# Performance work log

Hardware: AMD Instinct MI355X
Metric: run time of the kernel (lower is better)

## Reference

```python
import jax, jax.numpy as jnp
import numpy as np

# Arbitrary non-contiguous kernel tap offsets (constructor arg sk_ind)
SK_IND = np.array([-512, -256, -128, -96, -64, -48, -32, -24, -16, -12, -8, -6,
                   -4, -3, -2, -1, 0, 1, 2, 3, 4, 6, 8, 12, 16, 24, 32, 48,
                   64, 96, 128, 256], dtype=np.int32)
IN_CHANNELS = 64
OUT_CHANNELS = 64
BATCH = 16
INPUT_LEN = 4096


def setup_inputs() -> dict:
    key = jax.random.key(0)
    k1, k2 = jax.random.split(key)
    x = jax.random.normal(k1, (BATCH, IN_CHANNELS, INPUT_LEN), dtype=jnp.float32)
    sk_weights = jax.random.normal(k2, (OUT_CHANNELS, IN_CHANNELS, SK_IND.shape[0]), dtype=jnp.float32)
    return {"x": x, "sk_weights": sk_weights}


def reference(x, sk_weights):
    # x: [B, Cin, L]; sk_weights: [Cout, Cin, K]
    B, C, L = x.shape
    low_pad = max(-int(SK_IND.min()), 0)   # zeros consumed by negative taps
    high_pad = max(int(SK_IND.max()), 0)   # zeros consumed by positive taps
    # Original pads zeros AFTER the signal: [x, zeros(high_pad), zeros(low_pad)];
    # negative numpy indices then wrap into the trailing low_pad zeros.
    padded = jnp.concatenate([x, jnp.zeros((B, C, high_pad + low_pad), x.dtype)], axis=-1)
    padded_len = L + high_pad + low_pad
    idx = SK_IND[:, None] + np.arange(L)                 # [K, L], static
    idx = np.where(idx < 0, padded_len + idx, idx)       # emulate numpy negative-index wrap
    gathered = padded[:, :, idx]                          # [B, Cin, K, L]
    # Per-position GEMM: contract over (Cin, K)
    return jnp.einsum('oik,bikl->bol', sk_weights, gathered)  # [B, Cout, L]
```

## Files before the change

### kernel.cpp

```cpp
#include <hip/hip_runtime.h>


#define B_    16
#define CIN   64
#define COUT  64
#define LEN   4096
#define PAD_LO 512
#define PAD_HI 256
#define LPAD  (LEN + PAD_LO + PAD_HI)
#define NTAP  32

typedef float f32x4 __attribute__((ext_vector_type(4)));
typedef short bf16x8_s __attribute__((ext_vector_type(8)));
typedef __bf16 bf16x8_b __attribute__((ext_vector_type(8)));
typedef unsigned short u16x8 __attribute__((ext_vector_type(8)));

template <typename V>
static __device__ inline auto mfma_16x16x32_bf16(V a, V b, f32x4 c, int)
    -> decltype(__builtin_amdgcn_mfma_f32_16x16x32_bf16(a, b, c, 0, 0, 0)) {
  return __builtin_amdgcn_mfma_f32_16x16x32_bf16(a, b, c, 0, 0, 0);
}
template <typename V>
static __device__ inline f32x4 mfma_16x16x32_bf16(V a, V b, f32x4 c, long) {
  return __builtin_amdgcn_mfma_f32_16x16x32_bf16(
      __builtin_bit_cast(bf16x8_b, a), __builtin_bit_cast(bf16x8_b, b), c, 0, 0, 0);
}

static __device__ inline unsigned short f32_to_bf16_rne(float f) {
  unsigned int u = __builtin_bit_cast(unsigned int, f);
  u += 0x7fffu + ((u >> 16) & 1u);
  return (unsigned short)(u >> 16);
}

static __device__ inline void async_copy16(const void* g, void* l) {
  __builtin_amdgcn_global_load_lds((const __attribute__((address_space(1))) unsigned int*)g,
                                   (__attribute__((address_space(3))) unsigned int*)l, 16, 0, 0);
}

__global__ __launch_bounds__(256) void prep_xw(const float* __restrict__ x,
                                               const float* __restrict__ w,
                                               unsigned short* __restrict__ xp,
                                               unsigned short* __restrict__ wf) {
  __shared__ float tile[64][65];
  const int b = blockIdx.y;
  const int lp0 = blockIdx.x * 64;
  const int tid = threadIdx.x;
  const bool data = (lp0 >= PAD_LO) && (lp0 < PAD_LO + LEN);
  if (data) {
    const int l0 = lp0 - PAD_LO;
#pragma unroll
    for (int it = 0; it < 4; ++it) {
      const int pidx = it * 256 + tid;
      const int il = pidx >> 4;
      const int lq = (pidx & 15) * 4;
      const float4 v = *(const float4*)&x[(size_t)(b * CIN + il) * LEN + l0 + lq];
      tile[lq + 0][il] = v.x;
      tile[lq + 1][il] = v.y;
      tile[lq + 2][il] = v.z;
      tile[lq + 3][il] = v.w;
    }
  } else if (lp0 < PAD_LO) {
    const int base = (b * 8 + blockIdx.x) * 1024;
#pragma unroll
    for (int it = 0; it < 4; ++it) {
      const int e = base + it * 256 + tid;
      const int j = e & 7;
      const int lane = (e >> 3) & 63;
      const int m = (e >> 9) & 3;
      const int c = (e >> 11) & 1;
      const int t = e >> 12;
      const int o = m * 16 + (lane & 15);
      const int i = c * 32 + (lane >> 4) * 8 + j;
      wf[e] = f32_to_bf16_rne(w[(size_t)(o * CIN + i) * NTAP + t]);
    }
  }
  __syncthreads();
#pragma unroll
  for (int it = 0; it < 2; ++it) {
    const int pidx = it * 256 + tid;
    const int ll = pidx >> 3;
    const int i8 = (pidx & 7) * 8;
    u16x8 v = {0, 0, 0, 0, 0, 0, 0, 0};
    if (data) {
#pragma unroll
      for (int j = 0; j < 8; ++j) v[j] = f32_to_bf16_rne(tile[ll][i8 + j]);
    }
    *(u16x8*)&xp[(size_t)(b * LPAD + lp0 + ll) * CIN + i8] = v;
  }
}

__global__ __launch_bounds__(256, 2) void sconv_main(const unsigned short* __restrict__ xp,
                                                     const unsigned short* __restrict__ wf,
                                                     float* __restrict__ out) {
  constexpr int TAP[NTAP] = {-512, -256, -128, -96, -64, -48, -32, -24, -16, -12, -8,
                             -6,   -4,   -3,   -2,  -1,  0,   1,   2,   3,   4,  6,
                             8,    12,   16,   24,  32,  48,  64,  96,  128, 256};
  constexpr int NCH = 7;
  constexpr int CS[NCH + 1] = {0, 1, 2, 4, 8, 16, 24, 32};
  constexpr int SEND[NCH] = {-385, -129, 31, 103, 126, 135, 383};
  __shared__ alignas(16) char smem[65536];

  const int id = blockIdx.x;
  const int b = (id & 7) * 2 + ((id >> 3) & 1);
  const int l0 = (id >> 4) * 128;
  const int lb = l0 + PAD_LO;
  const int tid = threadIdx.x;
  const int wv = tid >> 6, lane = tid & 63;
  const int q = lane >> 4, r = lane & 15;
  const int lh = wv;

  const char* xbase = (const char*)xp + ((size_t)b * LPAD + lb) * (CIN * 2);
  const char* wbase = (const char*)wf;

  auto stageB = [&](int a0, int ng) {
    for (int g = wv; g < ng; g += 4) {
      const int ra = a0 + g * 8 + (lane >> 3);
      const int cs = (lane & 7) ^ (ra & 7);
      const int sb = (lb + a0 + g * 8) & 511;
      async_copy16(xbase + (ptrdiff_t)ra * 128 + cs * 16, smem + sb * 128);
    }
  };

  bf16x8_s Wreg[2][8], Breg[2][4];
  f32x4 acc[4][2] = {};

  auto loadW = [&](int tt, int p) {
    const char* src = wbase + tt * 8192 + lane * 16;
#pragma unroll
    for (int m = 0; m < 4; ++m)
#pragma unroll
      for (int c = 0; c < 2; ++c)
        Wreg[p][m * 2 + c] = *(const bf16x8_s*)(src + c * 4096 + m * 1024);
  };
  auto readB = [&](int tt, int p) {
    const int e = (TAP[tt] + r) & 7;
#pragma unroll
    for (int n = 0; n < 2; ++n) {
      const int slot = (lb + TAP[tt] + lh * 32 + 16 * n + r) & 511;
#pragma unroll
      for (int c = 0; c < 2; ++c)
        Breg[p][n * 2 + c] = *(const bf16x8_s*)(smem + slot * 128 + (((c * 4 + q) ^ e) << 4));
    }
  };

  loadW(0, 0);
  stageB(-512, 16);

#pragma unroll
  for (int i = 0; i < NCH; ++i) {
    __syncthreads();
    if (i + 1 < NCH) {
      const int ds = SEND[i] + 1;
      const int a0 = ds & ~7;
      stageB(a0, (SEND[i + 1] + 1 - a0 + 7) >> 3);
    }
    __builtin_amdgcn_sched_barrier(0);
    readB(CS[i], CS[i] & 1);
#pragma unroll
    for (int t = CS[i]; t < CS[i + 1]; ++t) {
      const int p = t & 1;
      if (t + 1 < NTAP) {
        loadW(t + 1, p ^ 1);
        if (t + 1 < CS[i + 1]) readB(t + 1, p ^ 1);
      }
      __builtin_amdgcn_sched_barrier(0);
#pragma unroll
      for (int c = 0; c < 2; ++c)
#pragma unroll
        for (int m = 0; m < 4; ++m)
#pragma unroll
          for (int n = 0; n < 2; ++n)
            acc[m][n] = mfma_16x16x32_bf16(Wreg[p][m * 2 + c], Breg[p][n * 2 + c], acc[m][n], 0);
    }
  }

#pragma unroll
  for (int m = 0; m < 4; ++m)
#pragma unroll
    for (int n = 0; n < 2; ++n)
#pragma unroll
      for (int d = 0; d < 4; ++d) {
        const int o = 16 * m + 4 * q + d;
        const int l = l0 + lh * 32 + 16 * n + r;
        out[((size_t)b * COUT + o) * LEN + l] = acc[m][n][d];
      }
}

extern "C" void kernel_launch(void* const* d_in, const int* in_sizes, int n_in,
                              void* d_out, int out_size, void* d_ws, size_t ws_size,
                              hipStream_t stream) {
  const float* x = (const float*)d_in[0];
  const float* w = (const float*)d_in[1];
  float* out = (float*)d_out;

  unsigned short* xp = (unsigned short*)d_ws;
  unsigned short* wfp = xp + (size_t)B_ * LPAD * CIN;

  prep_xw<<<dim3(LPAD / 64, B_), 256, 0, stream>>>(x, w, xp, wfp);
  sconv_main<<<dim3(16 * 32), 256, 0, stream>>>(xp, wfp, out);
}
```

Before: 92.30 us.

## Halve output tile per block and split channel reduction across waves

Each block now covers 64 output positions instead of 128, which doubles the grid to 1024 blocks. The four waves are split into two position halves times two input-channel halves. The two channel-half partial sums are reduced through shared memory before the store. The aim is more parallelism and fewer registers per wave, at the cost of an extra LDS reduction, two more barriers, and roughly double the redundant halo staging and weight reads per output.

```diff
diff --git a/kernel.cpp b/kernel.cpp
--- a/kernel.cpp
+++ b/kernel.cpp
@@ -97,17 +97,17 @@
                              8,    12,   16,   24,  32,  48,  64,  96,  128, 256};
   constexpr int NCH = 7;
   constexpr int CS[NCH + 1] = {0, 1, 2, 4, 8, 16, 24, 32};
-  constexpr int SEND[NCH] = {-385, -129, 31, 103, 126, 135, 383};
+  constexpr int SEND[NCH] = {-449, -193, -33, 39, 62, 75, 319};
   __shared__ alignas(16) char smem[65536];
 
   const int id = blockIdx.x;
-  const int b = (id & 7) * 2 + ((id >> 3) & 1);
-  const int l0 = (id >> 4) * 128;
+  const int b = (id & 7) * 2 + (id >> 9);
+  const int l0 = ((id >> 3) & 63) * 64;
   const int lb = l0 + PAD_LO;
   const int tid = threadIdx.x;
   const int wv = tid >> 6, lane = tid & 63;
   const int q = lane >> 4, r = lane & 15;
-  const int lh = wv;
+  const int lh = wv & 1, ch = wv >> 1;
 
   const char* xbase = (const char*)xp + ((size_t)b * LPAD + lb) * (CIN * 2);
   const char* wbase = (const char*)wf;
@@ -121,30 +121,26 @@
     }
   };
 
-  bf16x8_s Wreg[2][8], Breg[2][4];
+  bf16x8_s Wreg[2][4], Breg[2][2];
   f32x4 acc[4][2] = {};
 
   auto loadW = [&](int tt, int p) {
-    const char* src = wbase + tt * 8192 + lane * 16;
+    const char* src = wbase + tt * 8192 + ch * 4096 + lane * 16;
 #pragma unroll
     for (int m = 0; m < 4; ++m)
-#pragma unroll
-      for (int c = 0; c < 2; ++c)
-        Wreg[p][m * 2 + c] = *(const bf16x8_s*)(src + c * 4096 + m * 1024);
+      Wreg[p][m] = *(const bf16x8_s*)(src + m * 1024);
   };
   auto readB = [&](int tt, int p) {
     const int e = (TAP[tt] + r) & 7;
 #pragma unroll
     for (int n = 0; n < 2; ++n) {
       const int slot = (lb + TAP[tt] + lh * 32 + 16 * n + r) & 511;
-#pragma unroll
-      for (int c = 0; c < 2; ++c)
-        Breg[p][n * 2 + c] = *(const bf16x8_s*)(smem + slot * 128 + (((c * 4 + q) ^ e) << 4));
+      Breg[p][n] = *(const bf16x8_s*)(smem + slot * 128 + (((ch * 4 + q) ^ e) << 4));
     }
   };
 
   loadW(0, 0);
-  stageB(-512, 16);
+  stageB(-512, 8);
 
 #pragma unroll
   for (int i = 0; i < NCH; ++i) {
@@ -165,25 +161,37 @@
       }
       __builtin_amdgcn_sched_barrier(0);
 #pragma unroll
-      for (int c = 0; c < 2; ++c)
-#pragma unroll
-        for (int m = 0; m < 4; ++m)
-#pragma unroll
-          for (int n = 0; n < 2; ++n)
-            acc[m][n] = mfma_16x16x32_bf16(Wreg[p][m * 2 + c], Breg[p][n * 2 + c], acc[m][n], 0);
-    }
-  }
-
-#pragma unroll
-  for (int m = 0; m < 4; ++m)
-#pragma unroll
-    for (int n = 0; n < 2; ++n)
-#pragma unroll
-      for (int d = 0; d < 4; ++d) {
-        const int o = 16 * m + 4 * q + d;
-        const int l = l0 + lh * 32 + 16 * n + r;
-        out[((size_t)b * COUT + o) * LEN + l] = acc[m][n][d];
+      for (int m = 0; m < 4; ++m)
+#pragma unroll
+        for (int n = 0; n < 2; ++n)
+          acc[m][n] = mfma_16x16x32_bf16(Wreg[p][m], Breg[p][n], acc[m][n], 0);
+    }
+  }
+
+  __syncthreads();
+  if (ch == 1) {
+#pragma unroll
+    for (int m = 0; m < 4; ++m)
+#pragma unroll
+      for (int n = 0; n < 2; ++n)
+        *(f32x4*)(smem + lh * 8192 + ((m * 2 + n) * 64 + lane) * 16) = acc[m][n];
+  }
+  __syncthreads();
+  if (ch == 0) {
+#pragma unroll
+    for (int m = 0; m < 4; ++m)
+#pragma unroll
+      for (int n = 0; n < 2; ++n) {
+        const f32x4 other = *(const f32x4*)(smem + lh * 8192 + ((m * 2 + n) * 64 + lane) * 16);
+        const f32x4 v = acc[m][n] + other;
+#pragma unroll
+        for (int d = 0; d < 4; ++d) {
+          const int o = 16 * m + 4 * q + d;
+          const int l = l0 + lh * 32 + 16 * n + r;
+          out[((size_t)b * COUT + o) * LEN + l] = v[d];
+        }
       }
+  }
 }
 
 extern "C" void kernel_launch(void* const* d_in, const int* in_sizes, int n_in,
@@ -197,5 +205,5 @@
   unsigned short* wfp = xp + (size_t)B_ * LPAD * CIN;
 
   prep_xw<<<dim3(LPAD / 64, B_), 256, 0, stream>>>(x, w, xp, wfp);
-  sconv_main<<<dim3(16 * 32), 256, 0, stream>>>(xp, wfp, out);
-}
+  sconv_main<<<dim3(1024), 256, 0, stream>>>(xp, wfp, out);
+}
```

New measurement: 96.26 us. 1.04x slower.
